# Optimization experiments

Hardware: AMD Instinct MI355X
Metric: run time of the kernel (lower is better)

## Reference

```python
import jax, jax.numpy as jnp
import numpy as np

B, CIN, D, H, W = 2, 64, 16, 16, 16
CK, CV, COUT = 32, 64, 64
EPS = 1e-5


def setup_inputs() -> dict:
    key = jax.random.key(0)
    ks = jax.random.split(key, 11)
    return {
        "x": jax.random.normal(ks[0], (B, CIN, D, H, W), jnp.float32),
        "key_w": jax.random.normal(ks[1], (CK, CIN), jnp.float32) * 0.1,
        "bn_gamma": jax.random.uniform(ks[2], (CK,), jnp.float32, 0.5, 1.5),
        "bn_beta": jax.random.normal(ks[3], (CK,), jnp.float32) * 0.1,
        "bn_mean": jax.random.normal(ks[4], (CK,), jnp.float32) * 0.1,
        "bn_var": jax.random.uniform(ks[5], (CK,), jnp.float32, 0.5, 1.5),
        "value_w": jax.random.normal(ks[6], (CV, CIN), jnp.float32) * 0.1,
        "value_b": jax.random.normal(ks[7], (CV,), jnp.float32) * 0.1,
        "W_w": jax.random.normal(ks[8], (COUT, CV), jnp.float32) * 0.1,
        "W_b": jax.random.normal(ks[9], (COUT,), jnp.float32) * 0.1,
        "gamma": jax.random.normal(ks[10], (1,), jnp.float32),
    }


def reference(x, key_w, bn_gamma, bn_beta, bn_mean, bn_var,
              value_w, value_b, W_w, W_b, gamma):
    b, c, d, h, w = x.shape
    n = d * h * w
    xf = x.reshape(b, c, n)                       # [B, Cin, N]
    # f_key: 1x1x1 conv (no bias) + BatchNorm3d (eval mode, running stats)
    k = jnp.einsum('oc,bcn->bon', key_w, xf)      # [B, Ck, N]
    scale_bn = bn_gamma / jnp.sqrt(bn_var + EPS)
    k = (k - bn_mean[:, None]) * scale_bn[:, None] + bn_beta[:, None]
    # key_query_same=True -> query == key (same weights, same input)
    # f_value: 1x1x1 conv with bias
    v = jnp.einsum('oc,bcn->bon', value_w, xf) + value_b[:, None]  # [B, Cv, N]
    # sim_map = Q^T K scaled, softmax over last axis
    sim = jnp.einsum('bkn,bkm->bnm', k, k) * (CK ** -0.5)          # [B, N, N]
    sim = jax.nn.softmax(sim, axis=-1)
    # context = sim @ V^T  -> [B, N, Cv] -> [B, Cv, N]
    ctx = jnp.einsum('bnm,bvm->bvn', sim, v)
    # W: 1x1x1 conv
    ctx = jnp.einsum('ov,bvn->bon', W_w, ctx) + W_b[:, None]       # [B, Cout, N]
    ctx = ctx.reshape(b, COUT, d, h, w)
    # out_add=True branch: gamma * context + x
    return gamma.reshape(()) * ctx + x
```

## Files before the change

### kernel.cpp

```cpp
#include <hip/hip_runtime.h>
#include <hip/hip_bf16.h>
#include <math.h>

#define BATCH 2
#define CIN 64
#define NSP 4096
#define CK 32
#define CV 64
#define COUT 64
#define EPS 1e-5f
#define S4L 0.5050097680523077f

#define KB 64
#define NW 8
#define KPW (NSP / NW)
#define NCH (KPW / KB)

typedef unsigned short ushort_t;
using bf16x8 = __attribute__((ext_vector_type(8))) short;
using bf16x4 = __attribute__((ext_vector_type(4))) short;
using f32x4  = __attribute__((ext_vector_type(4))) float;
using float4_t = __attribute__((ext_vector_type(4))) float;

__device__ inline ushort_t f2bf(float f) {
  __hip_bfloat16 h = __float2bfloat16(f);
  return *reinterpret_cast<ushort_t*>(&h);
}

__global__ __launch_bounds__(512) void kv_kernel(
    const float* __restrict__ x,
    const float* __restrict__ key_w,
    const float* __restrict__ bn_gamma,
    const float* __restrict__ bn_beta,
    const float* __restrict__ bn_mean,
    const float* __restrict__ bn_var,
    const float* __restrict__ value_w,
    const float* __restrict__ value_b,
    ushort_t* __restrict__ KbT,
    ushort_t* __restrict__ Vbf) {
  __shared__ ushort_t XL[32][66];

  int tid = threadIdx.x, wid = tid >> 6, lane = tid & 63;
  int l15 = lane & 15, g = lane >> 4;
  int b  = blockIdx.x / (NSP / 32);
  int n0 = (blockIdx.x % (NSP / 32)) * 32;

  {
    int n = tid & 31, c4 = tid >> 5;
    const float* xb = x + ((size_t)b * CIN + c4 * 4) * NSP + n0 + n;
#pragma unroll
    for (int j = 0; j < 4; ++j)
      XL[n][c4 * 4 + j] = f2bf(xb[(size_t)j * NSP]);
  }
  __syncthreads();

  if (wid < 4) {
    int nsub = wid >> 1, osub = wid & 1;
    bf16x8 a[2];
#pragma unroll
    for (int kk = 0; kk < 2; ++kk)
      a[kk] = *(const bf16x8*)&XL[nsub * 16 + l15][kk * 32 + g * 8];
    bf16x8 bb[2];
#pragma unroll
    for (int kk = 0; kk < 2; ++kk) {
      const float* wp = key_w + (osub * 16 + l15) * CIN + kk * 32 + g * 8;
#pragma unroll
      for (int j = 0; j < 8; ++j) bb[kk][j] = (short)f2bf(wp[j]);
    }
    f32x4 d = {0.f, 0.f, 0.f, 0.f};
    d = __builtin_amdgcn_mfma_f32_16x16x32_bf16(a[0], bb[0], d, 0, 0, 0);
    d = __builtin_amdgcn_mfma_f32_16x16x32_bf16(a[1], bb[1], d, 0, 0, 0);
    int o = osub * 16 + l15;
    float sc  = bn_gamma[o] * rsqrtf(bn_var[o] + EPS);
    float scl = sc * S4L;
    float bi  = (bn_beta[o] - bn_mean[o] * sc) * S4L;
#pragma unroll
    for (int r = 0; r < 4; ++r) {
      int n = n0 + nsub * 16 + 4 * g + r;
      KbT[((size_t)b * NSP + n) * CK + o] = f2bf(d[r] * scl + bi);
    }
  } else {
    int osub = wid - 4;
    bf16x8 bbv[2][2];
#pragma unroll
    for (int nsub = 0; nsub < 2; ++nsub)
#pragma unroll
      for (int kk = 0; kk < 2; ++kk)
        bbv[nsub][kk] = *(const bf16x8*)&XL[nsub * 16 + l15][kk * 32 + g * 8];
    bf16x8 av[2];
#pragma unroll
    for (int kk = 0; kk < 2; ++kk) {
      const float* wp = value_w + (osub * 16 + l15) * CIN + kk * 32 + g * 8;
#pragma unroll
      for (int j = 0; j < 8; ++j) av[kk][j] = (short)f2bf(wp[j]);
    }
#pragma unroll
    for (int nsub = 0; nsub < 2; ++nsub) {
      f32x4 d = {0.f, 0.f, 0.f, 0.f};
      d = __builtin_amdgcn_mfma_f32_16x16x32_bf16(av[0], bbv[nsub][0], d, 0, 0, 0);
      d = __builtin_amdgcn_mfma_f32_16x16x32_bf16(av[1], bbv[nsub][1], d, 0, 0, 0);
#pragma unroll
      for (int r = 0; r < 4; ++r) {
        int o = osub * 16 + 4 * g + r;
        int n = n0 + nsub * 16 + l15;
        Vbf[((size_t)b * CV + o) * NSP + n] = f2bf(d[r] + value_b[o]);
      }
    }
  }
}

__global__ __launch_bounds__(512) void attn_proj_kernel(
    const ushort_t* __restrict__ KbT,
    const ushort_t* __restrict__ Vbf,
    const float* __restrict__ Ww,
    const float* __restrict__ Wb,
    const float* __restrict__ gamma,
    const float* __restrict__ x,
    float* __restrict__ out) {
  __shared__ __align__(16) ushort_t SMEM[NW * 8192];
  __shared__ __align__(16) float WL[COUT * CV];

  int tid = threadIdx.x, wid = tid >> 6, lane = tid & 63;
  int l15 = lane & 15, g = lane >> 4;
  int b  = blockIdx.x / (NSP / 32);
  int q0 = (blockIdx.x % (NSP / 32)) * 32;

  const ushort_t* Kb = KbT + (size_t)b * NSP * CK;
  const ushort_t* Vb = Vbf + (size_t)b * CV * NSP;

#pragma unroll
  for (int i = 0; i < 2; ++i) {
    size_t boff = (size_t)i * 8192 + wid * 1024;
    const float* src = (const float*)((const char*)Ww + boff + lane * 16);
    float* dst = (float*)((char*)WL + boff);
    __builtin_amdgcn_global_load_lds(
        (const __attribute__((address_space(1))) unsigned int*)src,
        (__attribute__((address_space(3))) unsigned int*)dst, 16, 0, 0);
  }

  bf16x8 qf[2];
#pragma unroll
  for (int qg = 0; qg < 2; ++qg)
    qf[qg] = *(const bf16x8*)&Kb[(size_t)(q0 + qg * 16 + l15) * CK + g * 8];
  asm volatile("s_waitcnt vmcnt(0)" ::: "memory");
  __builtin_amdgcn_sched_barrier(0);

  f32x4 acc[2][4];
  float Ssum[2] = {0.f, 0.f};
#pragma unroll
  for (int qg = 0; qg < 2; ++qg)
#pragma unroll
    for (int cg = 0; cg < 4; ++cg)
#pragma unroll
      for (int r = 0; r < 4; ++r) acc[qg][cg][r] = 0.f;

  int kbase = wid * KPW;

  auto stageK = [&](int buf, int n0k) {
    ushort_t* dstb = &SMEM[wid * 8192 + buf * 2048];
#pragma unroll
    for (int i = 0; i < 4; ++i) {
      int off = i * 1024 + lane * 16;
      int key = off >> 6;
      int c16 = (off >> 4) & 3;
      int sw  = c16 ^ ((key >> 1) & 3);
      const ushort_t* src = Kb + (size_t)(n0k + key) * CK + sw * 8;
      __builtin_amdgcn_global_load_lds(
          (const __attribute__((address_space(1))) unsigned int*)src,
          (__attribute__((address_space(3))) unsigned int*)&dstb[i * 512], 16, 0, 0);
    }
  };
  auto stageV = [&](int n0k) {
    ushort_t* dstb = &SMEM[wid * 8192 + 4096];
#pragma unroll
    for (int i = 0; i < 8; ++i) {
      int off = i * 1024 + lane * 16;
      int cv  = off >> 7;
      int c16 = (off >> 4) & 7;
      int sw  = c16 ^ (cv & 7);
      const ushort_t* src = Vb + (size_t)cv * NSP + n0k + sw * 8;
      __builtin_amdgcn_global_load_lds(
          (const __attribute__((address_space(1))) unsigned int*)src,
          (__attribute__((address_space(3))) unsigned int*)&dstb[i * 512], 16, 0, 0);
    }
  };

  stageK(0, kbase);
  stageV(kbase);
  stageK(1, kbase + KB);
  asm volatile("s_waitcnt vmcnt(12)" ::: "memory");
  __builtin_amdgcn_sched_barrier(0);

#pragma unroll
  for (int t = 0; t < NCH; ++t) {
    const ushort_t* KTc = &SMEM[wid * 8192 + (t & 1) * 2048];
    const ushort_t* VTc = &SMEM[wid * 8192 + 4096];

    bf16x8 kf[4];
#pragma unroll
    for (int kg = 0; kg < 4; ++kg) {
      int key = kg * 16 + l15;
      int sw  = g ^ ((key >> 1) & 3);
      kf[kg] = *(const bf16x8*)&KTc[key * CK + sw * 8];
    }
    f32x4 s[2][4];
    __builtin_amdgcn_s_setprio(1);
#pragma unroll
    for (int qg = 0; qg < 2; ++qg)
#pragma unroll
      for (int kg = 0; kg < 4; ++kg) {
        f32x4 z = {0.f, 0.f, 0.f, 0.f};
        s[qg][kg] = __builtin_amdgcn_mfma_f32_16x16x32_bf16(kf[kg], qf[qg], z, 0, 0, 0);
      }
    __builtin_amdgcn_s_setprio(0);

    float p[2][4][4];
#pragma unroll
    for (int qg = 0; qg < 2; ++qg)
#pragma unroll
      for (int kg = 0; kg < 4; ++kg) {
        float ps = 0.f;
#pragma unroll
        for (int r = 0; r < 4; ++r) {
          p[qg][kg][r] = exp2f(s[qg][kg][r]);
          ps += p[qg][kg][r];
        }
        Ssum[qg] += ps;
      }
    bf16x8 pa[2][2];
#pragma unroll
    for (int ks = 0; ks < 2; ++ks)
#pragma unroll
      for (int qg = 0; qg < 2; ++qg)
#pragma unroll
        for (int j = 0; j < 4; ++j) {
          pa[ks][qg][j]     = (short)f2bf(p[qg][2 * ks][j]);
          pa[ks][qg][4 + j] = (short)f2bf(p[qg][2 * ks + 1][j]);
        }

    if (t < NCH - 1) asm volatile("s_waitcnt vmcnt(4)" ::: "memory");
    else             asm volatile("s_waitcnt vmcnt(0)" ::: "memory");
    __builtin_amdgcn_sched_barrier(0);

    __builtin_amdgcn_s_setprio(1);
#pragma unroll
    for (int ks = 0; ks < 2; ++ks) {
#pragma unroll
      for (int cg = 0; cg < 4; ++cg) {
        int cv   = cg * 16 + l15;
        int x7   = cv & 7;
        int half = (g & 1) * 4;
        int t0   = (4 * ks + (g >> 1)) ^ x7;
        int t1   = (4 * ks + 2 + (g >> 1)) ^ x7;
        const ushort_t* vrow = &VTc[cv * KB];
        bf16x4 lo = *(const bf16x4*)&vrow[t0 * 8 + half];
        bf16x4 hi = *(const bf16x4*)&vrow[t1 * 8 + half];
        bf16x8 vf;
#pragma unroll
        for (int j = 0; j < 4; ++j) { vf[j] = lo[j]; vf[4 + j] = hi[j]; }
#pragma unroll
        for (int qg = 0; qg < 2; ++qg)
          acc[qg][cg] = __builtin_amdgcn_mfma_f32_16x16x32_bf16(pa[ks][qg], vf, acc[qg][cg], 0, 0, 0);
      }
    }
    __builtin_amdgcn_s_setprio(0);

    asm volatile("s_waitcnt lgkmcnt(0)" ::: "memory");
    __builtin_amdgcn_sched_barrier(0);

    if (t + 1 < NCH) stageV(kbase + (t + 1) * KB);
    if (t + 2 < NCH) stageK(t & 1, kbase + (t + 2) * KB);

    if (t + 2 < NCH)      asm volatile("s_waitcnt vmcnt(12)" ::: "memory");
    else if (t + 1 < NCH) asm volatile("s_waitcnt vmcnt(8)" ::: "memory");
    __builtin_amdgcn_sched_barrier(0);
  }

#pragma unroll
  for (int qg = 0; qg < 2; ++qg) {
    Ssum[qg] += __shfl_xor(Ssum[qg], 16, 64);
    Ssum[qg] += __shfl_xor(Ssum[qg], 32, 64);
  }

  __syncthreads();
  float* red = (float*)&SMEM[0];
  float* SsR = red + NW * 32 * 68;
#pragma unroll
  for (int qg = 0; qg < 2; ++qg) {
#pragma unroll
    for (int cg = 0; cg < 4; ++cg)
#pragma unroll
      for (int r = 0; r < 4; ++r) {
        int ql = qg * 16 + 4 * g + r;
        red[(wid * 32 + ql) * 68 + cg * 16 + l15] = acc[qg][cg][r];
      }
    if (g == 0) SsR[wid * 32 + qg * 16 + l15] = Ssum[qg];
  }
  __syncthreads();

  int n  = tid & 31;
  int sl = tid >> 5;
  {
    float4_t m4 = *(const float4_t*)&red[n * 68 + sl * 4];
#pragma unroll
    for (int w = 1; w < NW; ++w) {
      float4_t t4 = *(const float4_t*)&red[(w * 32 + n) * 68 + sl * 4];
      m4[0] += t4[0]; m4[1] += t4[1]; m4[2] += t4[2]; m4[3] += t4[3];
    }
    *(float4_t*)&red[n * 68 + sl * 4] = m4;
  }
  if (tid < 32) {
    float ds = 0.f;
#pragma unroll
    for (int w = 0; w < NW; ++w) ds += SsR[w * 32 + tid];
    SsR[tid] = ds;
  }
  __syncthreads();

  int og = tid >> 5;
  float invn = 1.f / SsR[n];

  float pacc[4];
#pragma unroll
  for (int j = 0; j < 4; ++j) pacc[j] = 0.f;
#pragma unroll
  for (int v4 = 0; v4 < 16; ++v4) {
    float4_t c4 = *(const float4_t*)&red[n * 68 + v4 * 4];
#pragma unroll
    for (int j = 0; j < 4; ++j) {
      float4_t w4 = *(const float4_t*)&WL[(og * 4 + j) * CV + v4 * 4];
      pacc[j] += w4[0] * c4[0] + w4[1] * c4[1] + w4[2] * c4[2] + w4[3] * c4[3];
    }
  }

  float gma = gamma[0];
#pragma unroll
  for (int j = 0; j < 4; ++j) {
    int o = og * 4 + j;
    size_t oi = ((size_t)b * COUT + o) * NSP + q0 + n;
    out[oi] = gma * (pacc[j] * invn + Wb[o]) + x[oi];
  }
}

extern "C" void kernel_launch(void* const* d_in, const int* in_sizes, int n_in,
                              void* d_out, int out_size, void* d_ws, size_t ws_size,
                              hipStream_t stream) {
  const float* x        = (const float*)d_in[0];
  const float* key_w    = (const float*)d_in[1];
  const float* bn_gamma = (const float*)d_in[2];
  const float* bn_beta  = (const float*)d_in[3];
  const float* bn_mean  = (const float*)d_in[4];
  const float* bn_var   = (const float*)d_in[5];
  const float* value_w  = (const float*)d_in[6];
  const float* value_b  = (const float*)d_in[7];
  const float* W_w      = (const float*)d_in[8];
  const float* W_b      = (const float*)d_in[9];
  const float* gamma    = (const float*)d_in[10];
  float* out = (float*)d_out;

  ushort_t* KbT = (ushort_t*)d_ws;
  ushort_t* Vbf = KbT + (size_t)BATCH * NSP * CK;

  kv_kernel<<<BATCH * (NSP / 32), 512, 0, stream>>>(
      x, key_w, bn_gamma, bn_beta, bn_mean, bn_var, value_w, value_b, KbT, Vbf);
  attn_proj_kernel<<<BATCH * (NSP / 32), 512, 0, stream>>>(
      KbT, Vbf, W_w, W_b, gamma, x, out);
}
```

Measured before the change: 28.33 us.

## Load V straight into double-buffered registers and halve LDS with two-phase reduction

V tiles are now read from global memory directly into a register double buffer instead of being staged through LDS with global_load_lds. This halves the per-block LDS allocation, which may allow a second block per CU, and removes the LDS write-then-read round trip for V. Because the smaller LDS region can no longer hold all eight waves' partial results, the cross-wave reduction becomes two phases: the upper four waves deposit their partials and the lower four accumulate them. The cost is higher VGPR pressure with possible spilling, narrower 8-byte global loads, and reliance on compiler-inserted vmcnt waits to order the K staging.

```diff
diff --git a/kernel.cpp b/kernel.cpp
--- a/kernel.cpp
+++ b/kernel.cpp
@@ -117,7 +117,7 @@
     const float* __restrict__ gamma,
     const float* __restrict__ x,
     float* __restrict__ out) {
-  __shared__ __align__(16) ushort_t SMEM[NW * 8192];
+  __shared__ __align__(16) ushort_t SMEM[NW * 4096];
   __shared__ __align__(16) float WL[COUT * CV];
 
   int tid = threadIdx.x, wid = tid >> 6, lane = tid & 63;
@@ -157,7 +157,7 @@
   int kbase = wid * KPW;
 
   auto stageK = [&](int buf, int n0k) {
-    ushort_t* dstb = &SMEM[wid * 8192 + buf * 2048];
+    ushort_t* dstb = &SMEM[wid * 4096 + buf * 2048];
 #pragma unroll
     for (int i = 0; i < 4; ++i) {
       int off = i * 1024 + lane * 16;
@@ -170,31 +170,29 @@
           (__attribute__((address_space(3))) unsigned int*)&dstb[i * 512], 16, 0, 0);
     }
   };
-  auto stageV = [&](int n0k) {
-    ushort_t* dstb = &SMEM[wid * 8192 + 4096];
-#pragma unroll
-    for (int i = 0; i < 8; ++i) {
-      int off = i * 1024 + lane * 16;
-      int cv  = off >> 7;
-      int c16 = (off >> 4) & 7;
-      int sw  = c16 ^ (cv & 7);
-      const ushort_t* src = Vb + (size_t)cv * NSP + n0k + sw * 8;
-      __builtin_amdgcn_global_load_lds(
-          (const __attribute__((address_space(1))) unsigned int*)src,
-          (__attribute__((address_space(3))) unsigned int*)&dstb[i * 512], 16, 0, 0);
-    }
+
+  bf16x4 vlo[2][2][4], vhi[2][2][4];
+  auto loadV = [&](int pb, int n0k) {
+#pragma unroll
+    for (int ks = 0; ks < 2; ++ks)
+#pragma unroll
+      for (int cg = 0; cg < 4; ++cg) {
+        const ushort_t* vr = Vb + (size_t)(cg * 16 + l15) * NSP + n0k + ks * 32 + 4 * g;
+        vlo[pb][ks][cg] = *(const bf16x4*)vr;
+        vhi[pb][ks][cg] = *(const bf16x4*)(vr + 16);
+      }
   };
 
   stageK(0, kbase);
-  stageV(kbase);
   stageK(1, kbase + KB);
-  asm volatile("s_waitcnt vmcnt(12)" ::: "memory");
+  loadV(0, kbase);
+  asm volatile("s_waitcnt vmcnt(20)" ::: "memory");
   __builtin_amdgcn_sched_barrier(0);
 
 #pragma unroll
   for (int t = 0; t < NCH; ++t) {
-    const ushort_t* KTc = &SMEM[wid * 8192 + (t & 1) * 2048];
-    const ushort_t* VTc = &SMEM[wid * 8192 + 4096];
+    const int cur = t & 1;
+    const ushort_t* KTc = &SMEM[wid * 4096 + cur * 2048];
 
     bf16x8 kf[4];
 #pragma unroll
@@ -238,26 +236,17 @@
           pa[ks][qg][4 + j] = (short)f2bf(p[qg][2 * ks + 1][j]);
         }
 
-    if (t < NCH - 1) asm volatile("s_waitcnt vmcnt(4)" ::: "memory");
-    else             asm volatile("s_waitcnt vmcnt(0)" ::: "memory");
-    __builtin_amdgcn_sched_barrier(0);
-
     __builtin_amdgcn_s_setprio(1);
 #pragma unroll
     for (int ks = 0; ks < 2; ++ks) {
 #pragma unroll
       for (int cg = 0; cg < 4; ++cg) {
-        int cv   = cg * 16 + l15;
-        int x7   = cv & 7;
-        int half = (g & 1) * 4;
-        int t0   = (4 * ks + (g >> 1)) ^ x7;
-        int t1   = (4 * ks + 2 + (g >> 1)) ^ x7;
-        const ushort_t* vrow = &VTc[cv * KB];
-        bf16x4 lo = *(const bf16x4*)&vrow[t0 * 8 + half];
-        bf16x4 hi = *(const bf16x4*)&vrow[t1 * 8 + half];
         bf16x8 vf;
 #pragma unroll
-        for (int j = 0; j < 4; ++j) { vf[j] = lo[j]; vf[4 + j] = hi[j]; }
+        for (int j = 0; j < 4; ++j) {
+          vf[j]     = vlo[cur][ks][cg][j];
+          vf[4 + j] = vhi[cur][ks][cg][j];
+        }
 #pragma unroll
         for (int qg = 0; qg < 2; ++qg)
           acc[qg][cg] = __builtin_amdgcn_mfma_f32_16x16x32_bf16(pa[ks][qg], vf, acc[qg][cg], 0, 0, 0);
@@ -268,12 +257,8 @@
     asm volatile("s_waitcnt lgkmcnt(0)" ::: "memory");
     __builtin_amdgcn_sched_barrier(0);
 
-    if (t + 1 < NCH) stageV(kbase + (t + 1) * KB);
-    if (t + 2 < NCH) stageK(t & 1, kbase + (t + 2) * KB);
-
-    if (t + 2 < NCH)      asm volatile("s_waitcnt vmcnt(12)" ::: "memory");
-    else if (t + 1 < NCH) asm volatile("s_waitcnt vmcnt(8)" ::: "memory");
-    __builtin_amdgcn_sched_barrier(0);
+    if (t + 2 < NCH) stageK(cur, kbase + (t + 2) * KB);
+    if (t + 1 < NCH) loadV(cur ^ 1, kbase + (t + 1) * KB);
   }
 
 #pragma unroll
@@ -284,17 +269,49 @@
 
   __syncthreads();
   float* red = (float*)&SMEM[0];
-  float* SsR = red + NW * 32 * 68;
-#pragma unroll
-  for (int qg = 0; qg < 2; ++qg) {
-#pragma unroll
-    for (int cg = 0; cg < 4; ++cg)
-#pragma unroll
-      for (int r = 0; r < 4; ++r) {
-        int ql = qg * 16 + 4 * g + r;
-        red[(wid * 32 + ql) * 68 + cg * 16 + l15] = acc[qg][cg][r];
-      }
-    if (g == 0) SsR[wid * 32 + qg * 16 + l15] = Ssum[qg];
+  float* SsR = red + 4 * 32 * 68;
+
+  if (wid >= 4) {
+    int w = wid - 4;
+#pragma unroll
+    for (int qg = 0; qg < 2; ++qg) {
+#pragma unroll
+      for (int cg = 0; cg < 4; ++cg)
+#pragma unroll
+        for (int r = 0; r < 4; ++r) {
+          int ql = qg * 16 + 4 * g + r;
+          red[(w * 32 + ql) * 68 + cg * 16 + l15] = acc[qg][cg][r];
+        }
+      if (g == 0) SsR[w * 32 + qg * 16 + l15] = Ssum[qg];
+    }
+  }
+  __syncthreads();
+  if (wid < 4) {
+#pragma unroll
+    for (int qg = 0; qg < 2; ++qg) {
+#pragma unroll
+      for (int cg = 0; cg < 4; ++cg)
+#pragma unroll
+        for (int r = 0; r < 4; ++r) {
+          int ql = qg * 16 + 4 * g + r;
+          acc[qg][cg][r] += red[(wid * 32 + ql) * 68 + cg * 16 + l15];
+        }
+      Ssum[qg] += SsR[wid * 32 + qg * 16 + l15];
+    }
+  }
+  __syncthreads();
+  if (wid < 4) {
+#pragma unroll
+    for (int qg = 0; qg < 2; ++qg) {
+#pragma unroll
+      for (int cg = 0; cg < 4; ++cg)
+#pragma unroll
+        for (int r = 0; r < 4; ++r) {
+          int ql = qg * 16 + 4 * g + r;
+          red[(wid * 32 + ql) * 68 + cg * 16 + l15] = acc[qg][cg][r];
+        }
+      if (g == 0) SsR[wid * 32 + qg * 16 + l15] = Ssum[qg];
+    }
   }
   __syncthreads();
 
@@ -303,7 +320,7 @@
   {
     float4_t m4 = *(const float4_t*)&red[n * 68 + sl * 4];
 #pragma unroll
-    for (int w = 1; w < NW; ++w) {
+    for (int w = 1; w < 4; ++w) {
       float4_t t4 = *(const float4_t*)&red[(w * 32 + n) * 68 + sl * 4];
       m4[0] += t4[0]; m4[1] += t4[1]; m4[2] += t4[2]; m4[3] += t4[3];
     }
@@ -312,7 +329,7 @@
   if (tid < 32) {
     float ds = 0.f;
 #pragma unroll
-    for (int w = 0; w < NW; ++w) ds += SsR[w * 32 + tid];
+    for (int w = 0; w < 4; ++w) ds += SsR[w * 32 + tid];
     SsR[tid] = ds;
   }
   __syncthreads();
```

After: 45.23 us. 59.7% more time.
